# Kernel tuning notes

Hardware: AMD Instinct MI355X
Metric: run time of the kernel (lower is better)

Reference implementation:

```python
import jax, jax.numpy as jnp
import numpy as np

STATE_DIM = 4
MEAS_DIM = 2
N_ADAPT = 10
HID = 128
DT = 0.1
Q0_VAR = 0.1 ** 2   # PROCESS_NOISE_STD**2
R_VAR = 0.5 ** 2    # MEAS_NOise_STD**2

F_MAT = jnp.array([[1, 0, DT, 0], [0, 1, 0, DT], [0, 0, 1, 0], [0, 0, 0, 1]], dtype=jnp.float32)
H_MAT = jnp.array([[1, 0, 0, 0], [0, 1, 0, 0]], dtype=jnp.float32)
Q0 = jnp.eye(STATE_DIM, dtype=jnp.float32) * Q0_VAR
R = jnp.eye(MEAS_DIM, dtype=jnp.float32) * R_VAR
I4 = jnp.eye(STATE_DIM, dtype=jnp.float32)


def setup_inputs() -> dict:
    key = jax.random.key(0)
    ks = jax.random.split(key, 8)
    B, T = 1024, 512
    s = 0.1
    return {
        "measurements": jax.random.normal(ks[0], (B, T, MEAS_DIM), jnp.float32),
        "Q_tilde": jnp.eye(STATE_DIM)[None].repeat(N_ADAPT, 0) * 0.001
                   + jax.random.normal(ks[1], (N_ADAPT, STATE_DIM, STATE_DIM), jnp.float32) * 0.001,
        "W_ih": jax.random.normal(ks[2], (4 * HID, MEAS_DIM), jnp.float32) * s,
        "W_hh": jax.random.normal(ks[3], (4 * HID, HID), jnp.float32) * s,
        "b_ih": jax.random.normal(ks[4], (4 * HID,), jnp.float32) * s,
        "b_hh": jax.random.normal(ks[5], (4 * HID,), jnp.float32) * s,
        "W_fc": jax.random.normal(ks[6], (N_ADAPT, HID), jnp.float32) * s,
        "b_fc": jax.random.normal(ks[7], (N_ADAPT,), jnp.float32) * s,
    }


def _nnakf(measurements, Q_tilde, W_ih, W_hh, b_ih, b_hh, W_fc, b_fc):
    B = measurements.shape[0]
    x0 = jnp.zeros((B, STATE_DIM), jnp.float32)
    P0 = jnp.broadcast_to(I4, (B, STATE_DIM, STATE_DIM))
    h0 = jnp.zeros((B, HID), jnp.float32)
    c0 = jnp.zeros((B, HID), jnp.float32)

    def step(carry, z):
        x, P, h, c = carry
        # predict
        x_pred = x @ F_MAT.T                                   # [B,4]
        P_pred0 = jnp.einsum('ij,bjk,lk->bil', F_MAT, P, F_MAT) + Q0
        innov = z - x_pred @ H_MAT.T                           # [B,2]
        S0 = jnp.einsum('ij,bjk,lk->bil', H_MAT, P_pred0, H_MAT) + R
        In = innov ** 2 / jnp.diagonal(S0, axis1=-2, axis2=-1)  # [B,2]
        # LSTM cell (torch gate order i,f,g,o)
        gates = In @ W_ih.T + b_ih + h @ W_hh.T + b_hh          # [B,4H]
        i_g, f_g, g_g, o_g = jnp.split(gates, 4, axis=-1)
        c = jax.nn.sigmoid(f_g) * c + jax.nn.sigmoid(i_g) * jnp.tanh(g_g)
        h = jax.nn.sigmoid(o_g) * jnp.tanh(c)
        sigma = jax.nn.sigmoid(h @ W_fc.T + b_fc)               # [B,N]
        Q_adapt = Q0 + jnp.einsum('bn,nij->bij', sigma, Q_tilde)
        P_pred = P_pred0 - Q0 + Q_adapt
        # update
        S = jnp.einsum('ij,bjk,lk->bil', H_MAT, P_pred, H_MAT) + R   # [B,2,2]
        PHt = jnp.einsum('bij,kj->bik', P_pred, H_MAT)               # [B,4,2]
        K = PHt @ jnp.linalg.inv(S)                                  # [B,4,2]
        x = x_pred + jnp.einsum('bij,bj->bi', K, innov)
        P = (I4 - K @ H_MAT) @ P_pred
        return (x, P, h, c), x

    zs = jnp.swapaxes(measurements, 0, 1)  # [T,B,2]
    _, xs = jax.lax.scan(step, (x0, P0, h0, c0), zs)
    return jnp.swapaxes(xs, 0, 1)          # [B,T,4]


def reference(measurements, Q_tilde, W_ih, W_hh, b_ih, b_hh, W_fc, b_fc):
    return _nnakf(measurements, Q_tilde, W_ih, W_hh, b_ih, b_hh, W_fc, b_fc)
```

## Files before the change

### kernel.cpp

```cpp
#include <hip/hip_runtime.h>
#include <stdint.h>


#define DTc  0.1f
#define Q0V  0.01f
#define RV   0.25f

typedef __bf16 bf16x8 __attribute__((ext_vector_type(8)));
typedef float  f32x4  __attribute__((ext_vector_type(4)));

__device__ __forceinline__ unsigned short f2bf(float f) {
    union { float f; unsigned int ui; } c; c.f = f;
    unsigned int u = c.ui;
    return (unsigned short)((u + 0x7FFFu + ((u >> 16) & 1u)) >> 16);
}
__device__ __forceinline__ bf16x8 cvt8(float4 a, float4 b) {
    union { unsigned short us[8]; bf16x8 v; } r;
    r.us[0] = f2bf(a.x); r.us[1] = f2bf(a.y); r.us[2] = f2bf(a.z); r.us[3] = f2bf(a.w);
    r.us[4] = f2bf(b.x); r.us[5] = f2bf(b.y); r.us[6] = f2bf(b.z); r.us[7] = f2bf(b.w);
    return r.v;
}
__device__ __forceinline__ float rcpf(float x)  { return __builtin_amdgcn_rcpf(x); }
__device__ __forceinline__ float sigmf(float x) { return rcpf(1.0f + __expf(-x)); }
__device__ __forceinline__ float tanhf_(float x){ return 1.0f - 2.0f * rcpf(__expf(2.0f * x) + 1.0f); }

#define QP_ROT2  0x4E
#define QP_BC0   0x00
#define QP_BC1   0x55
template<int CTRL>
__device__ __forceinline__ float dppf(float x) {
    return __builtin_bit_cast(float,
        __builtin_amdgcn_update_dpp(0, __builtin_bit_cast(int, x), CTRL, 0xF, 0xF, true));
}

__global__ __launch_bounds__(512, 2) void nnakf_kernel(
    const float* __restrict__ meas,
    const float* __restrict__ Qt,
    const float* __restrict__ Wih,
    const float* __restrict__ Whh,
    const float* __restrict__ bih,
    const float* __restrict__ bhh,
    const float* __restrict__ Wfc,
    const float* __restrict__ bfc,
    float* __restrict__ out)
{
    __shared__ float          meas_s[4 * 1024];
    __shared__ unsigned short hbuf[640];
    __shared__ float          sig_s[64];
    __shared__ float2         inbuf[4];

    const int tid  = threadIdx.x;
    const int w    = tid >> 6;
    const int lane = tid & 63;
    const int idx  = lane & 15;
    const int q    = lane >> 4;
    const int j    = lane & 3;
    const int bg0  = blockIdx.x * 4;
    const int hh   = w * 16 + idx;

    {
        const float4* g4 = (const float4*)(meas + (size_t)bg0 * 1024);
        float4* ms4 = (float4*)meas_s;
        for (int k = tid; k < 1024; k += 512) ms4[k] = g4[k];
    }

    bf16x8 wf[4][4];
    f32x4  biasC[4];
    float2 wihr[4];
    const float4* whh4 = (const float4*)Whh;
    #pragma unroll
    for (int g = 0; g < 4; ++g) {
        const int n = (g << 7) + hh;
        const float bb = bih[n] + bhh[n];
        biasC[g] = (f32x4){bb, bb, bb, bb};
        wihr[g] = ((const float2*)Wih)[n];
        #pragma unroll
        for (int s = 0; s < 4; ++s) {
            float4 u0 = whh4[n * 32 + s * 8 + q * 2];
            float4 u1 = whh4[n * 32 + s * 8 + q * 2 + 1];
            wf[g][s] = cvt8(u0, u1);
        }
    }
    bf16x8 fcf[4];
    #pragma unroll
    for (int s = 0; s < 4; ++s) {
        float4 u0 = make_float4(0.f, 0.f, 0.f, 0.f), u1 = u0;
        if (idx < 10) {
            u0 = ((const float4*)Wfc)[idx * 32 + s * 8 + q * 2];
            u1 = ((const float4*)Wfc)[idx * 32 + s * 8 + q * 2 + 1];
        }
        fcf[s] = cvt8(u0, u1);
    }
    const float bfc_r = (idx < 10) ? bfc[idx] : 0.0f;
    float qreg[10][4];
    #pragma unroll
    for (int n = 0; n < 10; ++n)
        #pragma unroll
        for (int r = 0; r < 4; ++r) qreg[n][r] = Qt[n * 16 + r * 4 + j];

    float P0 = (j == 0) ? 1.f : 0.f, P1 = (j == 1) ? 1.f : 0.f;
    float P2 = (j == 2) ? 1.f : 0.f, P3 = (j == 3) ? 1.f : 0.f;
    float x0 = 0.f, x1 = 0.f, x2 = 0.f, x3 = 0.f;
    float cst = 0.f;
    float ppc0, ppc1, ppc2, ppc3, xp0, xp1, inn0, inn1, In0, In1;
    f32x4 acc[4];

    #define PREDICT(TT)                                                          \
    {                                                                            \
        const float fp0 = P0 + DTc * P2, fp1 = P1 + DTc * P3;                    \
        const float d0 = dppf<QP_ROT2>(P0), d1 = dppf<QP_ROT2>(P1);              \
        const float d2 = dppf<QP_ROT2>(P2), d3 = dppf<QP_ROT2>(P3);              \
        const float fq0 = d0 + DTc * d2, fq1 = d1 + DTc * d3;                    \
        const bool jl2 = (j < 2);                                                \
        ppc0 = fp0 + (jl2 ? DTc * fq0 : 0.f) + ((j == 0) ? Q0V : 0.f);           \
        ppc1 = fp1 + (jl2 ? DTc * fq1 : 0.f) + ((j == 1) ? Q0V : 0.f);           \
        ppc2 = P2  + (jl2 ? DTc * d2  : 0.f) + ((j == 2) ? Q0V : 0.f);           \
        ppc3 = P3  + (jl2 ? DTc * d3  : 0.f) + ((j == 3) ? Q0V : 0.f);           \
        xp0 = x0 + DTc * x2; xp1 = x1 + DTc * x3;                                \
        const float2 zz = *(const float2*)&meas_s[q * 1024 + 2 * (TT)];          \
        inn0 = zz.x - xp0; inn1 = zz.y - xp1;                                    \
        const float s000 = dppf<QP_BC0>(ppc0) + RV;                              \
        const float s011 = dppf<QP_BC1>(ppc1) + RV;                              \
        In0 = inn0 * inn0 * rcpf(s000);                                          \
        In1 = inn1 * inn1 * rcpf(s011);                                          \
    }

    __syncthreads();

    if (w == 0) {
        PREDICT(0)
        if (idx == 0) inbuf[q] = make_float2(In0, In1);
    }
    #pragma unroll
    for (int g = 0; g < 4; ++g) acc[g] = biasC[g];

    __syncthreads();

    for (int t = 0; t < 512; ++t) {
        {
            const float2 inq = inbuf[q];
            float pre[4];
            #pragma unroll
            for (int g = 0; g < 4; ++g)
                pre[g] = acc[g][0] + inq.x * wihr[g].x + inq.y * wihr[g].y;
            const float cn = sigmf(pre[1]) * cst + sigmf(pre[0]) * tanhf_(pre[2]);
            const float hn = sigmf(pre[3]) * tanhf_(cn);
            cst = cn;
            hbuf[q * 160 + hh] = f2bf(hn);
        }
        __syncthreads();

        bf16x8 af[4];
        #pragma unroll
        for (int s = 0; s < 4; ++s)
            af[s] = __builtin_bit_cast(bf16x8,
                        *(const uint4*)&hbuf[(idx >> 2) * 160 + s * 32 + q * 8]);

        if (w == 0) {
            f32x4 f0 = (f32x4){0.f, 0.f, 0.f, 0.f};
            f32x4 f1 = (f32x4){0.f, 0.f, 0.f, 0.f};
            f0 = __builtin_amdgcn_mfma_f32_16x16x32_bf16(af[0], fcf[0], f0, 0, 0, 0);
            f1 = __builtin_amdgcn_mfma_f32_16x16x32_bf16(af[1], fcf[1], f1, 0, 0, 0);
            f0 = __builtin_amdgcn_mfma_f32_16x16x32_bf16(af[2], fcf[2], f0, 0, 0, 0);
            f1 = __builtin_amdgcn_mfma_f32_16x16x32_bf16(af[3], fcf[3], f1, 0, 0, 0);
            const f32x4 facc = f0 + f1;
            const float sg = sigmf(facc[0] + bfc_r);
            if (idx < 10) sig_s[q * 16 + idx] = sg;
        }

        #pragma unroll
        for (int g = 0; g < 4; ++g)
            acc[g] = __builtin_amdgcn_mfma_f32_16x16x32_bf16(af[0], wf[g][0], biasC[g], 0, 0, 0);
        #pragma unroll
        for (int s = 1; s < 4; ++s)
            #pragma unroll
            for (int g = 0; g < 4; ++g)
                acc[g] = __builtin_amdgcn_mfma_f32_16x16x32_bf16(af[s], wf[g][s], acc[g], 0, 0, 0);

        if (w == 0) {
            float sn[10];
            #pragma unroll
            for (int n = 0; n < 10; ++n) sn[n] = sig_s[q * 16 + n];
            float a0 = 0.f, a1 = 0.f, a2 = 0.f, a3 = 0.f;
            float e0 = 0.f, e1 = 0.f, e2 = 0.f, e3 = 0.f;
            #pragma unroll
            for (int n = 0; n < 5; ++n) {
                a0 += sn[n] * qreg[n][0]; a1 += sn[n] * qreg[n][1];
                a2 += sn[n] * qreg[n][2]; a3 += sn[n] * qreg[n][3];
            }
            #pragma unroll
            for (int n = 5; n < 10; ++n) {
                e0 += sn[n] * qreg[n][0]; e1 += sn[n] * qreg[n][1];
                e2 += sn[n] * qreg[n][2]; e3 += sn[n] * qreg[n][3];
            }
            const float pc0 = ppc0 + a0 + e0;
            const float pc1 = ppc1 + a1 + e1;
            const float pc2 = ppc2 + a2 + e2;
            const float pc3 = ppc3 + a3 + e3;
            const float ph00 = dppf<QP_BC0>(pc0), ph01 = dppf<QP_BC1>(pc0);
            const float ph10 = dppf<QP_BC0>(pc1), ph11 = dppf<QP_BC1>(pc1);
            const float ph20 = dppf<QP_BC0>(pc2), ph21 = dppf<QP_BC1>(pc2);
            const float ph30 = dppf<QP_BC0>(pc3), ph31 = dppf<QP_BC1>(pc3);
            const float s00 = ph00 + RV, s01 = ph01, s10 = ph10, s11 = ph11 + RV;
            const float rdet = rcpf(s00 * s11 - s01 * s10);
            const float u0 = rdet * (s11 * inn0 - s01 * inn1);
            const float u1 = rdet * (s00 * inn1 - s10 * inn0);
            x0 = xp0 + ph00 * u0 + ph01 * u1;
            x1 = xp1 + ph10 * u0 + ph11 * u1;
            x2 = x2  + ph20 * u0 + ph21 * u1;
            x3 = x3  + ph30 * u0 + ph31 * u1;
            const float w0r = rdet * (s11 * pc0 - s01 * pc1);
            const float w1r = rdet * (s00 * pc1 - s10 * pc0);
            P0 = pc0 - ph00 * w0r - ph01 * w1r;
            P1 = pc1 - ph10 * w0r - ph11 * w1r;
            P2 = pc2 - ph20 * w0r - ph21 * w1r;
            P3 = pc3 - ph30 * w0r - ph31 * w1r;
            if (idx == 0) {
                float4* o = (float4*)out;
                o[(size_t)(bg0 + q) * 512 + t] = make_float4(x0, x1, x2, x3);
            }
            const int tn = (t < 511) ? t + 1 : 511;
            PREDICT(tn)
            if (idx == 0) inbuf[q] = make_float2(In0, In1);
        }
        __syncthreads();
    }
}

extern "C" void kernel_launch(void* const* d_in, const int* in_sizes, int n_in,
                              void* d_out, int out_size, void* d_ws, size_t ws_size,
                              hipStream_t stream) {
    (void)in_sizes; (void)n_in; (void)out_size; (void)d_ws; (void)ws_size;
    nnakf_kernel<<<256, 512, 0, stream>>>(
        (const float*)d_in[0],
        (const float*)d_in[1],
        (const float*)d_in[2],
        (const float*)d_in[3],
        (const float*)d_in[4],
        (const float*)d_in[5],
        (const float*)d_in[6],
        (const float*)d_in[7],
        (float*)d_out);
}
```

Baseline: 488.7 us.

## Dedicate a separate wavefront to the Kalman update and reduce sigma·Q via DPP

Result: slower. 813.8 us (+66.5%).

```diff
diff --git a/kernel.cpp b/kernel.cpp
--- a/kernel.cpp
+++ b/kernel.cpp
@@ -27,13 +27,17 @@
 #define QP_ROT2  0x4E
 #define QP_BC0   0x00
 #define QP_BC1   0x55
+#define QP_BC2   0xAA
+#define QP_BC3   0xFF
+#define ROW_ROR4 0x124
+#define ROW_ROR8 0x128
 template<int CTRL>
 __device__ __forceinline__ float dppf(float x) {
     return __builtin_bit_cast(float,
         __builtin_amdgcn_update_dpp(0, __builtin_bit_cast(int, x), CTRL, 0xF, 0xF, true));
 }
 
-__global__ __launch_bounds__(512, 2) void nnakf_kernel(
+__global__ __launch_bounds__(576, 1) void nnakf_kernel(
     const float* __restrict__ meas,
     const float* __restrict__ Qt,
     const float* __restrict__ Wih,
@@ -46,7 +50,6 @@
 {
     __shared__ float          meas_s[4 * 1024];
     __shared__ unsigned short hbuf[640];
-    __shared__ float          sig_s[64];
     __shared__ float2         inbuf[4];
 
     const int tid  = threadIdx.x;
@@ -55,13 +58,15 @@
     const int idx  = lane & 15;
     const int q    = lane >> 4;
     const int j    = lane & 3;
+    const int a4   = idx >> 2;
     const int bg0  = blockIdx.x * 4;
-    const int hh   = w * 16 + idx;
+    const int wl   = (w == 0) ? 0 : (w - 1);
+    const int hh   = wl * 16 + idx;
 
     {
         const float4* g4 = (const float4*)(meas + (size_t)bg0 * 1024);
         float4* ms4 = (float4*)meas_s;
-        for (int k = tid; k < 1024; k += 512) ms4[k] = g4[k];
+        for (int k = tid; k < 1024; k += 576) ms4[k] = g4[k];
     }
 
     bf16x8 wf[4][4];
@@ -92,11 +97,14 @@
         fcf[s] = cvt8(u0, u1);
     }
     const float bfc_r = (idx < 10) ? bfc[idx] : 0.0f;
-    float qreg[10][4];
-    #pragma unroll
-    for (int n = 0; n < 10; ++n)
+    float qreg2[4][4];
+    #pragma unroll
+    for (int c = 0; c < 4; ++c) {
+        const int n = 4 * a4 + c;
         #pragma unroll
-        for (int r = 0; r < 4; ++r) qreg[n][r] = Qt[n * 16 + r * 4 + j];
+        for (int r = 0; r < 4; ++r)
+            qreg2[c][r] = (n < 10) ? Qt[n * 16 + r * 4 + j] : 0.0f;
+    }
 
     float P0 = (j == 0) ? 1.f : 0.f, P1 = (j == 1) ? 1.f : 0.f;
     float P2 = (j == 2) ? 1.f : 0.f, P3 = (j == 3) ? 1.f : 0.f;
@@ -137,7 +145,7 @@
     __syncthreads();
 
     for (int t = 0; t < 512; ++t) {
-        {
+        if (w > 0) {
             const float2 inq = inbuf[q];
             float pre[4];
             #pragma unroll
@@ -164,39 +172,24 @@
             f0 = __builtin_amdgcn_mfma_f32_16x16x32_bf16(af[2], fcf[2], f0, 0, 0, 0);
             f1 = __builtin_amdgcn_mfma_f32_16x16x32_bf16(af[3], fcf[3], f1, 0, 0, 0);
             const f32x4 facc = f0 + f1;
-            const float sg = sigmf(facc[0] + bfc_r);
-            if (idx < 10) sig_s[q * 16 + idx] = sg;
-        }
-
-        #pragma unroll
-        for (int g = 0; g < 4; ++g)
-            acc[g] = __builtin_amdgcn_mfma_f32_16x16x32_bf16(af[0], wf[g][0], biasC[g], 0, 0, 0);
-        #pragma unroll
-        for (int s = 1; s < 4; ++s)
-            #pragma unroll
-            for (int g = 0; g < 4; ++g)
-                acc[g] = __builtin_amdgcn_mfma_f32_16x16x32_bf16(af[s], wf[g][s], acc[g], 0, 0, 0);
-
-        if (w == 0) {
-            float sn[10];
-            #pragma unroll
-            for (int n = 0; n < 10; ++n) sn[n] = sig_s[q * 16 + n];
-            float a0 = 0.f, a1 = 0.f, a2 = 0.f, a3 = 0.f;
-            float e0 = 0.f, e1 = 0.f, e2 = 0.f, e3 = 0.f;
-            #pragma unroll
-            for (int n = 0; n < 5; ++n) {
-                a0 += sn[n] * qreg[n][0]; a1 += sn[n] * qreg[n][1];
-                a2 += sn[n] * qreg[n][2]; a3 += sn[n] * qreg[n][3];
-            }
-            #pragma unroll
-            for (int n = 5; n < 10; ++n) {
-                e0 += sn[n] * qreg[n][0]; e1 += sn[n] * qreg[n][1];
-                e2 += sn[n] * qreg[n][2]; e3 += sn[n] * qreg[n][3];
-            }
-            const float pc0 = ppc0 + a0 + e0;
-            const float pc1 = ppc1 + a1 + e1;
-            const float pc2 = ppc2 + a2 + e2;
-            const float pc3 = ppc3 + a3 + e3;
+            const float sg = (idx < 10) ? sigmf(facc[0] + bfc_r) : 0.0f;
+
+            const float s0 = dppf<QP_BC0>(sg), s1 = dppf<QP_BC1>(sg);
+            const float s2 = dppf<QP_BC2>(sg), s3 = dppf<QP_BC3>(sg);
+            float p0 = s0 * qreg2[0][0] + s1 * qreg2[1][0] + s2 * qreg2[2][0] + s3 * qreg2[3][0];
+            float p1 = s0 * qreg2[0][1] + s1 * qreg2[1][1] + s2 * qreg2[2][1] + s3 * qreg2[3][1];
+            float p2 = s0 * qreg2[0][2] + s1 * qreg2[1][2] + s2 * qreg2[2][2] + s3 * qreg2[3][2];
+            float p3 = s0 * qreg2[0][3] + s1 * qreg2[1][3] + s2 * qreg2[2][3] + s3 * qreg2[3][3];
+            p0 += dppf<ROW_ROR4>(p0); p1 += dppf<ROW_ROR4>(p1);
+            p2 += dppf<ROW_ROR4>(p2); p3 += dppf<ROW_ROR4>(p3);
+            p0 += dppf<ROW_ROR8>(p0); p1 += dppf<ROW_ROR8>(p1);
+            p2 += dppf<ROW_ROR8>(p2); p3 += dppf<ROW_ROR8>(p3);
+
+            const float pc0 = ppc0 + p0;
+            const float pc1 = ppc1 + p1;
+            const float pc2 = ppc2 + p2;
+            const float pc3 = ppc3 + p3;
+
             const float ph00 = dppf<QP_BC0>(pc0), ph01 = dppf<QP_BC1>(pc0);
             const float ph10 = dppf<QP_BC0>(pc1), ph11 = dppf<QP_BC1>(pc1);
             const float ph20 = dppf<QP_BC0>(pc2), ph21 = dppf<QP_BC1>(pc2);
@@ -222,6 +215,15 @@
             const int tn = (t < 511) ? t + 1 : 511;
             PREDICT(tn)
             if (idx == 0) inbuf[q] = make_float2(In0, In1);
+        } else {
+            #pragma unroll
+            for (int g = 0; g < 4; ++g)
+                acc[g] = __builtin_amdgcn_mfma_f32_16x16x32_bf16(af[0], wf[g][0], biasC[g], 0, 0, 0);
+            #pragma unroll
+            for (int s = 1; s < 4; ++s)
+                #pragma unroll
+                for (int g = 0; g < 4; ++g)
+                    acc[g] = __builtin_amdgcn_mfma_f32_16x16x32_bf16(af[s], wf[g][s], acc[g], 0, 0, 0);
         }
         __syncthreads();
     }
@@ -231,7 +233,7 @@
                               void* d_out, int out_size, void* d_ws, size_t ws_size,
                               hipStream_t stream) {
     (void)in_sizes; (void)n_in; (void)out_size; (void)d_ws; (void)ws_size;
-    nnakf_kernel<<<256, 512, 0, stream>>>(
+    nnakf_kernel<<<256, 576, 0, stream>>>(
         (const float*)d_in[0],
         (const float*)d_in[1],
         (const float*)d_in[2],
```
